# Performance work log

Hardware: AMD Instinct MI355X
Metric: run time of the kernel (lower is better)

## Reference

```python
import jax, jax.numpy as jnp
import numpy as np

N_NODES = 50000
N_EDGES = 800000
IN_DIM = 128
HEAD = 4
HD = 16  # output_dim per head


def setup_inputs() -> dict:
    key = jax.random.key(0)
    k_h, k_src, k_dst, k_ww, k_bw, k_wa, k_ba = jax.random.split(key, 7)
    h = jax.random.normal(k_h, (N_NODES, IN_DIM), dtype=jnp.float32)
    src = jax.random.randint(k_src, (N_EDGES,), 0, N_NODES, dtype=jnp.int32)
    dst = jax.random.randint(k_dst, (N_EDGES,), 0, N_NODES, dtype=jnp.int32)
    # w_linear: Linear(input_dim, output_dim*head)
    W_w = jax.random.normal(k_ww, (IN_DIM, HEAD * HD), dtype=jnp.float32) / np.sqrt(IN_DIM)
    b_w = jax.random.normal(k_bw, (HEAD * HD,), dtype=jnp.float32) * 0.01
    # atten: Linear(2*hd, 1), shared across heads
    W_a = jax.random.normal(k_wa, (2 * HD, 1), dtype=jnp.float32) / np.sqrt(2 * HD)
    b_a = jax.random.normal(k_ba, (1,), dtype=jnp.float32) * 0.01
    return {"h": h, "W_w": W_w, "b_w": b_w, "W_a": W_a, "b_a": b_a,
            "src": src, "dst": dst}


def reference(h, W_w, b_w, W_a, b_a, src, dst):
    # Node projection: g.ndata['h'] = w_linear(h)  -> [N, head*hd]
    hw = (h @ W_w + b_w).reshape(-1, HEAD, HD)          # [N, head, hd]
    sf = hw[src]                                         # [E, head, hd] src features
    df = hw[dst]                                         # [E, head, hd] dst features
    z = jnp.concatenate([sf, df], axis=-1)               # [E, head, 2*hd]
    alpha = (z @ W_a + b_a)[..., 0]                      # [E, head]
    alpha = jax.nn.leaky_relu(alpha, negative_slope=0.01)
    # Mailbox softmax over incoming edges per (dst node, head) = segment softmax
    m = jax.ops.segment_max(alpha, dst, num_segments=N_NODES)   # [N, head]
    e = jnp.exp(alpha - m[dst])                                 # [E, head]
    denom = jax.ops.segment_sum(e, dst, num_segments=N_NODES)   # [N, head]
    w = e / denom[dst]                                          # [E, head]
    # Weighted sum of src features scattered to dst
    out = jax.ops.segment_sum(w[..., None] * sf, dst, num_segments=N_NODES)  # [N, head, hd]
    return out.reshape(-1, HEAD * HD)  # if_sum=False path
```

## Files before the change

kernel.cpp:

```cpp
#include <hip/hip_runtime.h>

#define BINW 32
#define CAP  768
#define EPB  8192
#define SLOT 24
#define MAXBINS 2048

__device__ __forceinline__ unsigned pack_bf16x2(float x, float y) {
    unsigned ux = __float_as_uint(x); ux += 0x7fffu + ((ux >> 16) & 1);
    unsigned uy = __float_as_uint(y); uy += 0x7fffu + ((uy >> 16) & 1);
    return (ux >> 16) | (uy & 0xffff0000u);
}

__global__ __launch_bounds__(256) void k_s1(
    const float* __restrict__ h, const float* __restrict__ Ww,
    const float* __restrict__ bw, const float* __restrict__ Wa,
    const float* __restrict__ ba_p,
    const int* __restrict__ src, const int* __restrict__ dst,
    unsigned short* __restrict__ hw16,
    float* __restrict__ asrc, float* __restrict__ adst,
    int* __restrict__ percnt, unsigned* __restrict__ binned,
    int n_nodes, int n_edges, int nbins, int nbb)
{
    const int t = threadIdx.x;
    if ((int)blockIdx.x < nbb) {
        __shared__ int cursor[MAXBINS];
        const int bb = blockIdx.x;
        for (int i = t; i < nbins; i += 256) cursor[i] = 0;
        __syncthreads();
#pragma unroll
        for (int half = 0; half < 2; ++half) {
            const int e0 = bb * EPB + half * (EPB / 2);
            unsigned myw[16]; int myr[16];
#pragma unroll
            for (int k = 0; k < 16; ++k) {
                int e = e0 + k * 256 + t;
                myw[k] = 0xffffffffu;
                if (e < n_edges) {
                    int d = dst[e], s = src[e];
                    int b = d >> 5;
                    myw[k] = ((unsigned)b << 21) | ((unsigned)s << 5) | (unsigned)(d & 31);
                    myr[k] = atomicAdd(&cursor[b], 1);
                }
            }
#pragma unroll
            for (int k = 0; k < 16; ++k) {
                unsigned w = myw[k];
                if (w != 0xffffffffu && myr[k] < SLOT) {
                    int b = w >> 21;
                    binned[((unsigned)b * nbb + bb) * SLOT + myr[k]] = w & 0x1fffffu;
                }
            }
        }
        __syncthreads();
        for (int i = t; i < nbins; i += 256)
            percnt[bb * nbins + i] = min(cursor[i], SLOT);
        return;
    }
    __shared__ float ws[128 * 64];
#pragma unroll
    for (int i = 0; i < 8; ++i)
        ((float4*)ws)[i * 256 + t] = ((const float4*)Ww)[i * 256 + t];
    __syncthreads();

    const int bid  = (int)blockIdx.x - nbb;
    const int lane = t & 63;
    const int wid  = t >> 6;
    const int cg   = lane & 15;
    const int rsub = lane >> 4;
    const int head = cg >> 2;
    const int row0 = (bid * 4 + wid) * 16 + rsub * 4;
    if (row0 >= n_nodes) return;

    float acc[4][4];
#pragma unroll
    for (int r = 0; r < 4; ++r)
#pragma unroll
        for (int c = 0; c < 4; ++c) acc[r][c] = 0.f;

    const float* hrow = h + (size_t)row0 * 128;

    for (int k = 0; k < 128; k += 4) {
        float ha[4][4];
#pragma unroll
        for (int r = 0; r < 4; ++r)
            *(float4*)ha[r] = *(const float4*)(hrow + r * 128 + k);
#pragma unroll
        for (int kk = 0; kk < 4; ++kk) {
            float4 w4 = *(const float4*)(&ws[(k + kk) * 64 + cg * 4]);
#pragma unroll
            for (int r = 0; r < 4; ++r) {
                acc[r][0] = __fmaf_rn(ha[r][kk], w4.x, acc[r][0]);
                acc[r][1] = __fmaf_rn(ha[r][kk], w4.y, acc[r][1]);
                acc[r][2] = __fmaf_rn(ha[r][kk], w4.z, acc[r][2]);
                acc[r][3] = __fmaf_rn(ha[r][kk], w4.w, acc[r][3]);
            }
        }
    }
    const float4 b4 = *(const float4*)(bw + cg * 4);
    const int j0 = (cg & 3) * 4;
    const float4 waS = *(const float4*)(Wa + j0);
    const float4 waD = *(const float4*)(Wa + 16 + j0);
    const float ba = *ba_p;
#pragma unroll
    for (int r = 0; r < 4; ++r) {
        float4 o;
        o.x = acc[r][0] + b4.x;
        o.y = acc[r][1] + b4.y;
        o.z = acc[r][2] + b4.z;
        o.w = acc[r][3] + b4.w;
        const size_t idx = (size_t)(row0 + r) * 64 + cg * 4;
        uint2 p;
        p.x = pack_bf16x2(o.x, o.y);
        p.y = pack_bf16x2(o.z, o.w);
        *(uint2*)(hw16 + idx) = p;

        float pas = o.x * waS.x + o.y * waS.y + o.z * waS.z + o.w * waS.w;
        float pad = o.x * waD.x + o.y * waD.y + o.z * waD.z + o.w * waD.w;
        pas += __shfl_xor(pas, 1);
        pas += __shfl_xor(pas, 2);
        pad += __shfl_xor(pad, 1);
        pad += __shfl_xor(pad, 2);
        if ((cg & 3) == 0) {
            asrc[(row0 + r) * 4 + head] = pas;
            adst[(row0 + r) * 4 + head] = pad + ba;
        }
    }
}

__global__ __launch_bounds__(512) void k_gather(
    const int* __restrict__ percnt, const unsigned* __restrict__ binned,
    const float* __restrict__ asrc, const float* __restrict__ adst,
    const unsigned short* __restrict__ hw16, float* __restrict__ out,
    int n_nodes, int nbins, int nbb)
{
    __shared__ int seg_off[136];
    __shared__ unsigned data[CAP], srt[CAP];
    __shared__ float ebuf[CAP * 4];
    __shared__ int hist[BINW], lstart[BINW];
    const int t = threadIdx.x;
    const int b = blockIdx.x;
    const int lane = t & 63;
    const int wid  = t >> 6;

    if (t < BINW) hist[t] = 0;
    if (t >= 64 && t < 128) {
        const int tt = t - 64;
        int carry = 0;
        for (int base = 0; base < nbb; base += 64) {
            int i = base + tt;
            int v = (i < nbb) ? percnt[i * nbins + b] : 0;
            int x = v;
#pragma unroll
            for (int off = 1; off < 64; off <<= 1) {
                int n_ = __shfl_up(x, off);
                if (tt >= off) x += n_;
            }
            if (i < nbb) seg_off[i] = carry + x - v;
            carry += __shfl(x, 63);
        }
        if (tt == 0) seg_off[nbb] = carry;
    }
    __syncthreads();
    const int cnt = min(seg_off[nbb], CAP);

    const int half = lane >> 5;
    const int sl   = lane & 31;
    for (int bb0 = wid * 2 + half; bb0 < nbb; bb0 += 16) {
        int o0 = seg_off[bb0];
        int c  = seg_off[bb0 + 1] - o0;
        if (sl < c && o0 + sl < CAP) {
            unsigned w = binned[((unsigned)b * nbb + bb0) * SLOT + sl];
            unsigned r = (unsigned)atomicAdd(&hist[w & 31], 1);
            data[o0 + sl] = w | (r << 21);
        }
    }
    __syncthreads();
    if (t < BINW) {
        int v = hist[t];
        int x = v;
#pragma unroll
        for (int off = 1; off < BINW; off <<= 1) {
            int n_ = __shfl_up(x, off);
            if (t >= off) x += n_;
        }
        lstart[t] = x - v;
    }
    __syncthreads();
    for (int i = t; i < cnt; i += 512) {
        unsigned w = data[i];
        int pos = lstart[w & 31] + (int)(w >> 21);
        srt[pos] = w;
        int s  = (int)((w >> 5) & 0xffffu);
        int dl = (int)(w & 31u);
        float4 av = *(const float4*)(asrc + (unsigned)s * 4);
        float4 dv = *(const float4*)(adst + (unsigned)(b * BINW + dl) * 4);
        float a0 = av.x + dv.x; a0 = fmaxf(a0, 0.01f * a0);
        float a1 = av.y + dv.y; a1 = fmaxf(a1, 0.01f * a1);
        float a2 = av.z + dv.z; a2 = fmaxf(a2, 0.01f * a2);
        float a3 = av.w + dv.w; a3 = fmaxf(a3, 0.01f * a3);
        float4 ev;
        ev.x = __expf(a0); ev.y = __expf(a1); ev.z = __expf(a2); ev.w = __expf(a3);
        *(float4*)(ebuf + (unsigned)pos * 4) = ev;
    }
    __syncthreads();

    const int head = lane >> 4;

    for (int j = 0; j < 4; ++j) {
        const int dlow = wid + 8 * j;
        const int d = b * BINW + dlow;
        if (d >= n_nodes) continue;
        const int start = lstart[dlow];
        const int cd = hist[dlow];
        if (cd <= 0) {
            out[(size_t)d * 64 + lane] = 0.f;
            continue;
        }
        const int end = start + cd;
        float acc = 0.f, den = 0.f;

        for (int i = start; i < end; i += 8) {
#pragma unroll
            for (int k = 0; k < 8; ++k) {
                int idx = i + k;
                int ld = (idx < end) ? idx : start;
                unsigned w = srt[ld];
                float ea = ebuf[(unsigned)ld * 4 + head];
                ea = (idx < end) ? ea : 0.f;
                int s = (int)((w >> 5) & 0xffffu);
                float hv = __uint_as_float((unsigned)hw16[(unsigned)(s * 64 + lane)] << 16);
                den += ea;
                acc = __fmaf_rn(ea, hv, acc);
            }
        }
        out[(size_t)d * 64 + lane] = acc / den;
    }
}

extern "C" void kernel_launch(void* const* d_in, const int* in_sizes, int n_in,
                              void* d_out, int out_size, void* d_ws, size_t ws_size,
                              hipStream_t stream)
{
    const float* h  = (const float*)d_in[0];
    const float* Ww = (const float*)d_in[1];
    const float* bw = (const float*)d_in[2];
    const float* Wa = (const float*)d_in[3];
    const float* ba = (const float*)d_in[4];
    const int* src  = (const int*)d_in[5];
    const int* dst  = (const int*)d_in[6];

    const int n_nodes = in_sizes[0] / 128;
    const int n_edges = in_sizes[5];
    const int nbins = (n_nodes + BINW - 1) / BINW;
    const int nbb   = (n_edges + EPB - 1) / EPB;

    unsigned short* hw16 = (unsigned short*)d_ws;
    float* asrc          = (float*)(hw16 + (size_t)n_nodes * 64);
    float* adst          = asrc + (size_t)n_nodes * 4;
    int* percnt          = (int*)(adst + (size_t)n_nodes * 4);
    unsigned* binned     = (unsigned*)(percnt + (size_t)nbb * nbins);

    float* out = (float*)d_out;

    const int proj_blocks = (n_nodes + 63) / 64;
    k_s1<<<nbb + proj_blocks, 256, 0, stream>>>(
        h, Ww, bw, Wa, ba, src, dst, hw16, asrc, adst, percnt, binned,
        n_nodes, n_edges, nbins, nbb);

    k_gather<<<nbins, 512, 0, stream>>>(
        percnt, binned, asrc, adst, hw16, out, n_nodes, nbins, nbb);
}
```

Before: 66.00 us.

## Shrink projection tile to two rows, prefetch h, union shared memory

The projection blocks now compute two rows per thread instead of four, which doubles the number of projection blocks, and they software-prefetch the next h float4 chunk while computing the current one. The binning cursor array and the weight tile now share one shared-memory union, so each block allocates only the larger of the two. The aim is lower register and LDS use per block, giving higher occupancy and better latency hiding on the memory-bound projection. In exchange, each block reloads the 32KB weight tile for half as many rows, which doubles the global-to-shared weight traffic.

```diff
diff --git a/kernel.cpp b/kernel.cpp
--- a/kernel.cpp
+++ b/kernel.cpp
@@ -11,6 +11,11 @@
     unsigned uy = __float_as_uint(y); uy += 0x7fffu + ((uy >> 16) & 1);
     return (ux >> 16) | (uy & 0xffff0000u);
 }
+
+union SMem1 {
+    float ws[128 * 64];
+    int cursor[MAXBINS];
+};
 
 __global__ __launch_bounds__(256) void k_s1(
     const float* __restrict__ h, const float* __restrict__ Ww,
@@ -22,11 +27,11 @@
     int* __restrict__ percnt, unsigned* __restrict__ binned,
     int n_nodes, int n_edges, int nbins, int nbb)
 {
+    __shared__ SMem1 u;
     const int t = threadIdx.x;
     if ((int)blockIdx.x < nbb) {
-        __shared__ int cursor[MAXBINS];
         const int bb = blockIdx.x;
-        for (int i = t; i < nbins; i += 256) cursor[i] = 0;
+        for (int i = t; i < nbins; i += 256) u.cursor[i] = 0;
         __syncthreads();
 #pragma unroll
         for (int half = 0; half < 2; ++half) {
@@ -40,7 +45,7 @@
                     int d = dst[e], s = src[e];
                     int b = d >> 5;
                     myw[k] = ((unsigned)b << 21) | ((unsigned)s << 5) | (unsigned)(d & 31);
-                    myr[k] = atomicAdd(&cursor[b], 1);
+                    myr[k] = atomicAdd(&u.cursor[b], 1);
                 }
             }
 #pragma unroll
@@ -54,13 +59,12 @@
         }
         __syncthreads();
         for (int i = t; i < nbins; i += 256)
-            percnt[bb * nbins + i] = min(cursor[i], SLOT);
+            percnt[bb * nbins + i] = min(u.cursor[i], SLOT);
         return;
     }
-    __shared__ float ws[128 * 64];
 #pragma unroll
     for (int i = 0; i < 8; ++i)
-        ((float4*)ws)[i * 256 + t] = ((const float4*)Ww)[i * 256 + t];
+        ((float4*)u.ws)[i * 256 + t] = ((const float4*)Ww)[i * 256 + t];
     __syncthreads();
 
     const int bid  = (int)blockIdx.x - nbb;
@@ -69,33 +73,40 @@
     const int cg   = lane & 15;
     const int rsub = lane >> 4;
     const int head = cg >> 2;
-    const int row0 = (bid * 4 + wid) * 16 + rsub * 4;
+    const int row0 = (bid * 4 + wid) * 8 + rsub * 2;
     if (row0 >= n_nodes) return;
 
-    float acc[4][4];
-#pragma unroll
-    for (int r = 0; r < 4; ++r)
+    float acc[2][4];
+#pragma unroll
+    for (int r = 0; r < 2; ++r)
 #pragma unroll
         for (int c = 0; c < 4; ++c) acc[r][c] = 0.f;
 
     const float* hrow = h + (size_t)row0 * 128;
 
+    float4 ha0 = *(const float4*)(hrow);
+    float4 ha1 = *(const float4*)(hrow + 128);
     for (int k = 0; k < 128; k += 4) {
-        float ha[4][4];
-#pragma unroll
-        for (int r = 0; r < 4; ++r)
-            *(float4*)ha[r] = *(const float4*)(hrow + r * 128 + k);
+        float4 hb0, hb1;
+        if (k + 4 < 128) {
+            hb0 = *(const float4*)(hrow + k + 4);
+            hb1 = *(const float4*)(hrow + 128 + k + 4);
+        }
+        const float* a0 = (const float*)&ha0;
+        const float* a1 = (const float*)&ha1;
 #pragma unroll
         for (int kk = 0; kk < 4; ++kk) {
-            float4 w4 = *(const float4*)(&ws[(k + kk) * 64 + cg * 4]);
-#pragma unroll
-            for (int r = 0; r < 4; ++r) {
-                acc[r][0] = __fmaf_rn(ha[r][kk], w4.x, acc[r][0]);
-                acc[r][1] = __fmaf_rn(ha[r][kk], w4.y, acc[r][1]);
-                acc[r][2] = __fmaf_rn(ha[r][kk], w4.z, acc[r][2]);
-                acc[r][3] = __fmaf_rn(ha[r][kk], w4.w, acc[r][3]);
-            }
-        }
+            float4 w4 = *(const float4*)(&u.ws[(k + kk) * 64 + cg * 4]);
+            acc[0][0] = __fmaf_rn(a0[kk], w4.x, acc[0][0]);
+            acc[0][1] = __fmaf_rn(a0[kk], w4.y, acc[0][1]);
+            acc[0][2] = __fmaf_rn(a0[kk], w4.z, acc[0][2]);
+            acc[0][3] = __fmaf_rn(a0[kk], w4.w, acc[0][3]);
+            acc[1][0] = __fmaf_rn(a1[kk], w4.x, acc[1][0]);
+            acc[1][1] = __fmaf_rn(a1[kk], w4.y, acc[1][1]);
+            acc[1][2] = __fmaf_rn(a1[kk], w4.z, acc[1][2]);
+            acc[1][3] = __fmaf_rn(a1[kk], w4.w, acc[1][3]);
+        }
+        ha0 = hb0; ha1 = hb1;
     }
     const float4 b4 = *(const float4*)(bw + cg * 4);
     const int j0 = (cg & 3) * 4;
@@ -103,7 +114,7 @@
     const float4 waD = *(const float4*)(Wa + 16 + j0);
     const float ba = *ba_p;
 #pragma unroll
-    for (int r = 0; r < 4; ++r) {
+    for (int r = 0; r < 2; ++r) {
         float4 o;
         o.x = acc[r][0] + b4.x;
         o.y = acc[r][1] + b4.y;
@@ -263,7 +274,7 @@
 
     float* out = (float*)d_out;
 
-    const int proj_blocks = (n_nodes + 63) / 64;
+    const int proj_blocks = (n_nodes + 31) / 32;
     k_s1<<<nbb + proj_blocks, 256, 0, stream>>>(
         h, Ww, bw, Wa, ba, src, dst, hw16, asrc, adst, percnt, binned,
         n_nodes, n_edges, nbins, nbb);
```

Result: slower. 242.7 us (+267.8%).
